# Kernel tuning notes

Measured on AMD Instinct MI355X. Metric: run time of the kernel, lower is better.

The kernel has to match this reference:

```python
import jax, jax.numpy as jnp
import numpy as np

N, E, H, Q, M, B, L = 100000, 800000, 64, 4, 8, 100, 4
EPS_BN = 1e-5


def setup_inputs() -> dict:
    key = jax.random.key(0)
    ki = iter(jax.random.split(key, 32))
    def nrm(shape, scale=1.0):
        return jax.random.normal(next(ki), shape, dtype=jnp.float32) * scale
    inp = {}
    inp["x"] = nrm((N, H))
    inp["pe"] = nrm((N, Q, M, 2))
    inp["Lam"] = jax.random.uniform(next(ki), (B, Q, M), jnp.float32, 0.0, 2.0)
    inp["edge_attr"] = nrm((E, H))
    # per-layer eigenvalue MLP phi: scalar -> 16 -> scalar
    inp["phi_w1"] = nrm((L, 1, 16))
    inp["phi_b1"] = jnp.zeros((L, 16), jnp.float32)
    inp["phi_w2"] = nrm((L, 16, 1), 0.25)
    inp["phi_b2"] = jnp.zeros((L, 1), jnp.float32)
    # per-layer edge PE encoder linear: [2*Q*M -> H]
    inp["enc_w"] = nrm((L, 2 * Q * M, H), (2.0 / (2 * Q * M)) ** 0.5)
    inp["enc_b"] = jnp.zeros((L, H), jnp.float32)
    # per-layer GINE edge linear
    inp["lin_w"] = nrm((L, H, H), (2.0 / H) ** 0.5)
    inp["lin_b"] = jnp.zeros((L, H), jnp.float32)
    # per-layer GINE MLP: Linear -> BN -> ReLU -> Linear
    inp["mlp_w1"] = nrm((L, H, H), (2.0 / H) ** 0.5)
    inp["mlp_b1"] = jnp.zeros((L, H), jnp.float32)
    inp["bn1_g"] = jnp.ones((L, H), jnp.float32)
    inp["bn1_b"] = jnp.zeros((L, H), jnp.float32)
    inp["mlp_w2"] = nrm((L, H, H), (2.0 / H) ** 0.5)
    inp["mlp_b2"] = jnp.zeros((L, H), jnp.float32)
    # per-layer outer BatchNorm
    inp["bn2_g"] = jnp.ones((L, H), jnp.float32)
    inp["bn2_b"] = jnp.zeros((L, H), jnp.float32)
    inp["edge_index"] = jax.random.randint(next(ki), (2, E), 0, N, dtype=jnp.int32)
    inp["batch"] = jnp.sort(jax.random.randint(next(ki), (N,), 0, B, dtype=jnp.int32))
    return inp


def _bn(h, g, b):
    # training-mode BatchNorm1d over the node/row axis
    mu = h.mean(axis=0)
    var = h.var(axis=0)
    return (h - mu) * jax.lax.rsqrt(var + EPS_BN) * g + b


def _forward(x, pe, Lam, edge_attr, params, edge_index, batch):
    (phi_w1, phi_b1, phi_w2, phi_b2, enc_w, enc_b, lin_w, lin_b,
     mlp_w1, mlp_b1, bn1_g, bn1_b, mlp_w2, mlp_b2, bn2_g, bn2_b) = params
    src, dst = edge_index[0], edge_index[1]
    # permutation-invariant complex edge features: pe[src] * conj(pe[dst]), per (q, eigvec)
    zs_re, zs_im = pe[src, ..., 0], pe[src, ..., 1]   # [E, Q, M]
    zd_re, zd_im = pe[dst, ..., 0], pe[dst, ..., 1]
    z_re = zs_re * zd_re + zs_im * zd_im              # [E, Q, M]
    z_im = zs_im * zd_re - zs_re * zd_im
    eg = batch[src]                                    # graph id per edge  [E]
    for l in range(L):
        # eigenvalue MLP -> per-eigenvector weight  [B, Q, M]
        hphi = jax.nn.relu(Lam[..., None] @ phi_w1[l] + phi_b1[l])   # [B,Q,M,16]
        w = (hphi @ phi_w2[l])[..., 0] + phi_b2[l][0]                # [B,Q,M]
        we = w[eg]                                                   # [E,Q,M]
        feat = jnp.concatenate([(z_re * we).reshape(E, Q * M),
                                (z_im * we).reshape(E, Q * M)], axis=-1)  # [E, 2QM]
        edge_pe = feat @ enc_w[l] + enc_b[l]                          # [E,H]
        ea = edge_pe + edge_attr
        # GINE message: ReLU(x_j + lin(edge_attr)), sum-aggregated at dst
        msg = jax.nn.relu(x[src] + ea @ lin_w[l] + lin_b[l])          # [E,H]
        agg = jax.ops.segment_sum(msg, dst, num_segments=N)           # [N,H]
        h = x + agg                                                   # (1+eps)*x with eps=0
        h = jax.nn.relu(_bn(h @ mlp_w1[l] + mlp_b1[l], bn1_g[l], bn1_b[l]))
        h = h @ mlp_w2[l] + mlp_b2[l]
        x = _bn(h, bn2_g[l], bn2_b[l])
        if l != L - 1:
            x = jax.nn.relu(x)
    return x


def reference(x, pe, Lam, edge_attr, phi_w1, phi_b1, phi_w2, phi_b2, enc_w, enc_b,
              lin_w, lin_b, mlp_w1, mlp_b1, bn1_g, bn1_b, mlp_w2, mlp_b2, bn2_g, bn2_b,
              edge_index, batch):
    params = (phi_w1, phi_b1, phi_w2, phi_b2, enc_w, enc_b, lin_w, lin_b,
              mlp_w1, mlp_b1, bn1_g, bn1_b, mlp_w2, mlp_b2, bn2_g, bn2_b)
    return (_forward(x, pe, Lam, edge_attr, params, edge_index, batch), pe)
```

## Files before the change

kernel.cpp:

```cpp
#include <hip/hip_runtime.h>

#define N_NODES 100000
#define N_EDGES 800000
#define NB 100
#define NL 4
#define QM 32
#define EPS_BN 1e-5f

typedef __bf16 bf16_t;
typedef __bf16 bf16x8 __attribute__((ext_vector_type(8)));
typedef __bf16 bf16x4 __attribute__((ext_vector_type(4)));
typedef __bf16 bf16x2 __attribute__((ext_vector_type(2)));
typedef float f32x4 __attribute__((ext_vector_type(4)));


__global__ void k_count(const int* __restrict__ dst, int* __restrict__ counts) {
    int e = blockIdx.x * 256 + threadIdx.x;
    if (e < N_EDGES) atomicAdd(&counts[dst[e]], 1);
}

__global__ void k_scan1(const int* __restrict__ counts, int* __restrict__ row_ptr,
                        int* __restrict__ blk) {
    __shared__ int s[1024];
    int i = blockIdx.x * 1024 + threadIdx.x;
    int v = (i < N_NODES) ? counts[i] : 0;
    s[threadIdx.x] = v;
    __syncthreads();
    for (int off = 1; off < 1024; off <<= 1) {
        int u = (threadIdx.x >= off) ? s[threadIdx.x - off] : 0;
        __syncthreads();
        s[threadIdx.x] += u;
        __syncthreads();
    }
    if (i < N_NODES) row_ptr[i] = s[threadIdx.x] - v;
    if (threadIdx.x == 1023) blk[blockIdx.x] = s[1023];
}

__global__ void k_scan2(int* __restrict__ blk) {
    __shared__ int s[128];
    int t = threadIdx.x;
    int v = (t < 98) ? blk[t] : 0;
    s[t] = v;
    __syncthreads();
    for (int off = 1; off < 128; off <<= 1) {
        int u = (t >= off) ? s[t - off] : 0;
        __syncthreads();
        s[t] += u;
        __syncthreads();
    }
    if (t < 98) blk[t] = s[t] - v;
}

__global__ void k_scan3(const int* __restrict__ blk, int* __restrict__ row_ptr) {
    int i = blockIdx.x * 1024 + threadIdx.x;
    if (i < N_NODES) row_ptr[i] += blk[blockIdx.x];
    if (i == 0) row_ptr[N_NODES] = N_EDGES;
}

__global__ void k_scatter(const int* __restrict__ ei, const int* __restrict__ batch,
                          const int* __restrict__ row_ptr, int* __restrict__ cursor,
                          int4* __restrict__ edat) {
    int e = blockIdx.x * 256 + threadIdx.x;
    if (e >= N_EDGES) return;
    int s = ei[e], d = ei[N_EDGES + e];
    int pos = row_ptr[d] + atomicAdd(&cursor[d], 1);
    edat[pos] = make_int4(s, d, batch[s], e);
}

__global__ void k_permute(const float* __restrict__ pe, const float* __restrict__ ea,
                          const int4* __restrict__ edat, bf16_t* __restrict__ feat) {
    int t = blockIdx.x * 256 + threadIdx.x;
    int p = t >> 4, k = t & 15;
    int4 ed = edat[p];
    int src = ed.x, dst = ed.y, e = ed.w;
    f32x4 av = *(const f32x4*)(ea + (size_t)e * 64 + k * 4);
    bf16x4 ao;
#pragma unroll
    for (int i = 0; i < 4; i++) ao[i] = (bf16_t)av[i];
    *(bf16x4*)(feat + (size_t)p * 128 + 64 + k * 4) = ao;
    f32x4 sv = *(const f32x4*)(pe + (size_t)src * 64 + k * 4);
    f32x4 dv = *(const f32x4*)(pe + (size_t)dst * 64 + k * 4);
    bf16x2 re, im;
    re[0] = (bf16_t)(sv[0] * dv[0] + sv[1] * dv[1]);
    re[1] = (bf16_t)(sv[2] * dv[2] + sv[3] * dv[3]);
    im[0] = (bf16_t)(sv[1] * dv[0] - sv[0] * dv[1]);
    im[1] = (bf16_t)(sv[3] * dv[2] - sv[2] * dv[3]);
    *(bf16x2*)(feat + (size_t)p * 128 + 2 * k) = re;
    *(bf16x2*)(feat + (size_t)p * 128 + 32 + 2 * k) = im;
}


__global__ void k_phi(const float* __restrict__ Lam, const float* __restrict__ w1,
                      const float* __restrict__ b1, const float* __restrict__ w2,
                      const float* __restrict__ b2, bf16_t* __restrict__ w_all) {
    int idx = blockIdx.x * 256 + threadIdx.x;
    if (idx >= NL * NB * QM) return;
    int l = idx / (NB * QM);
    int rem = idx % (NB * QM);
    float lam = Lam[rem];
    float acc = b2[l];
    for (int i = 0; i < 16; i++) {
        float h = lam * w1[l * 16 + i] + b1[l * 16 + i];
        acc += fmaxf(h, 0.f) * w2[l * 16 + i];
    }
    w_all[idx] = (bf16_t)acc;
}

__global__ void k_prep(const float* __restrict__ enc_w, const float* __restrict__ enc_b,
                       const float* __restrict__ lin_w, const float* __restrict__ lin_b,
                       const float* __restrict__ mlp_w1, const float* __restrict__ mlp_w2,
                       bf16_t* __restrict__ wcat_frag, bf16_t* __restrict__ w1frag,
                       bf16_t* __restrict__ w2frag, float* __restrict__ cvec) {
    __shared__ float lds[128][64];
    int l = blockIdx.x, tid = threadIdx.x;
    const float* ew = enc_w + l * 64 * 64;
    const float* lw = lin_w + l * 64 * 64;
    for (int idx = tid; idx < 64 * 64; idx += 256) {
        int r = idx >> 6, c = idx & 63;
        float acc = 0.f;
        for (int k = 0; k < 64; k++) acc += ew[r * 64 + k] * lw[k * 64 + c];
        lds[r][c] = acc;
        lds[64 + r][c] = lw[r * 64 + c];
    }
    if (tid < 64) {
        float acc = lin_b[l * 64 + tid];
        for (int k = 0; k < 64; k++) acc += enc_b[l * 64 + k] * lw[k * 64 + tid];
        cvec[l * 64 + tid] = acc;
    }
    __syncthreads();
    for (int idx = tid; idx < 16 * 512; idx += 256) {
        int sn = idx >> 9, lane = (idx >> 3) & 63, j = idx & 7;
        int s = sn >> 2, nt = sn & 3;
        int row = 32 * s + (lane >> 4) * 8 + j;
        int col = 16 * nt + (lane & 15);
        wcat_frag[l * 8192 + idx] = (bf16_t)lds[row][col];
    }
    for (int idx = tid; idx < 8 * 512; idx += 256) {
        int sn = idx >> 9, lane = (idx >> 3) & 63, j = idx & 7;
        int s = sn >> 2, nt = sn & 3;
        int row = 32 * s + (lane >> 4) * 8 + j;
        int col = 16 * nt + (lane & 15);
        w1frag[l * 4096 + idx] = (bf16_t)mlp_w1[(l * 64 + row) * 64 + col];
        w2frag[l * 4096 + idx] = (bf16_t)mlp_w2[(l * 64 + row) * 64 + col];
    }
}


__global__ void k_hinit0(const float* __restrict__ x, bf16_t* __restrict__ x_bf,
                         float* __restrict__ h) {
    size_t i = ((size_t)blockIdx.x * 256 + threadIdx.x) * 8;
    f32x4 a = *(const f32x4*)(x + i), b = *(const f32x4*)(x + i + 4);
    *(f32x4*)(h + i) = a;
    *(f32x4*)(h + i + 4) = b;
    bf16x8 o;
#pragma unroll
    for (int k = 0; k < 4; k++) { o[k] = (bf16_t)a[k]; o[k + 4] = (bf16_t)b[k]; }
    *(bf16x8*)(x_bf + i) = o;
}

__global__ void k_edge(const bf16_t* __restrict__ feat, const int4* __restrict__ edat,
                       const int* __restrict__ row_ptr, const bf16_t* __restrict__ w_l,
                       const bf16_t* __restrict__ wcat_l, const float* __restrict__ cvec_l,
                       const bf16_t* __restrict__ x_bf, float* __restrict__ h) {
    __shared__ float msg[128][68];
    int tid = threadIdx.x;
    int wave = tid >> 6, lane = tid & 63;
    int quad = lane >> 4, l16 = lane & 15;
    int e0 = blockIdx.x * 128;

    bf16x8 bfrag[4][4];
    const bf16x8* wf = (const bf16x8*)wcat_l;
#pragma unroll
    for (int s = 0; s < 4; s++)
#pragma unroll
        for (int nt = 0; nt < 4; nt++) bfrag[s][nt] = wf[(s * 4 + nt) * 64 + lane];

    f32x4 acc[2][4];
#pragma unroll
    for (int rt = 0; rt < 2; rt++)
#pragma unroll
        for (int nt = 0; nt < 4; nt++) acc[rt][nt] = (f32x4)(0.f);

    int em[2];
    bf16x8 wch[2];
#pragma unroll
    for (int rt = 0; rt < 2; rt++) {
        em[rt] = e0 + wave * 32 + rt * 16 + l16;
        int eg = edat[em[rt]].z;
        wch[rt] = *(const bf16x8*)(w_l + (size_t)eg * QM + quad * 8);
    }
#pragma unroll
    for (int s = 0; s < 4; s++) {
        bf16x8 afr[2];
#pragma unroll
        for (int rt = 0; rt < 2; rt++) {
            bf16x8 v = *(const bf16x8*)(feat + (size_t)em[rt] * 128 + s * 32 + quad * 8);
            if (s < 2) {
                bf16x8 a;
#pragma unroll
                for (int i = 0; i < 8; i++) a[i] = (bf16_t)((float)v[i] * (float)wch[rt][i]);
                afr[rt] = a;
            } else {
                afr[rt] = v;
            }
        }
#pragma unroll
        for (int rt = 0; rt < 2; rt++)
#pragma unroll
            for (int nt = 0; nt < 4; nt++)
                acc[rt][nt] = __builtin_amdgcn_mfma_f32_16x16x32_bf16(afr[rt], bfrag[s][nt],
                                                                     acc[rt][nt], 0, 0, 0);
    }
#pragma unroll
    for (int nt = 0; nt < 4; nt++) {
        float cv = cvec_l[nt * 16 + l16];
#pragma unroll
        for (int rt = 0; rt < 2; rt++)
#pragma unroll
            for (int r = 0; r < 4; r++)
                msg[wave * 32 + rt * 16 + quad * 4 + r][nt * 16 + l16] = acc[rt][nt][r] + cv;
    }
    __syncthreads();
#pragma unroll
    for (int it = 0; it < 4; it++) {
        int j = it * 32 + (tid >> 3);
        int l8 = tid & 7;
        int srcn = edat[e0 + j].x;
        bf16x8 xv = *(const bf16x8*)(x_bf + (size_t)srcn * 64 + l8 * 8);
        float* mrow = &msg[j][l8 * 8];
        f32x4 m0 = *(const f32x4*)mrow, m1 = *(const f32x4*)(mrow + 4);
#pragma unroll
        for (int k = 0; k < 4; k++) {
            m0[k] = fmaxf(m0[k] + (float)xv[k], 0.f);
            m1[k] = fmaxf(m1[k] + (float)xv[k + 4], 0.f);
        }
        *(f32x4*)mrow = m0;
        *(f32x4*)(mrow + 4) = m1;
    }
    __syncthreads();
    int nfirst = edat[e0].y, nlast = edat[e0 + 127].y;
    int c = tid & 63;
    for (int n = nfirst + (tid >> 6); n <= nlast; n += 4) {
        int rs = row_ptr[n], re = row_ptr[n + 1];
        int a = rs > e0 ? rs : e0;
        int b = re < e0 + 128 ? re : e0 + 128;
        if (a >= b) continue;
        float sum = 0.f;
        for (int jj = a; jj < b; jj++) sum += msg[jj - e0][c];
        float* addr = h + (size_t)n * 64 + c;
        if (rs >= e0 && re <= e0 + 128) *addr += sum;
        else atomicAdd(addr, sum);
    }
}

__global__ void k_mlp1(const float* __restrict__ h, const bf16_t* __restrict__ w1frag_l,
                       const float* __restrict__ b1_l, bf16_t* __restrict__ t,
                       float* __restrict__ stats) {
    __shared__ float sred[128];
    int tid = threadIdx.x, wave = tid >> 6, lane = tid & 63, quad = lane >> 4, l16 = lane & 15;
    int r0 = blockIdx.x * 128;
    bf16x8 bfrag[2][4];
    const bf16x8* wf = (const bf16x8*)w1frag_l;
#pragma unroll
    for (int s = 0; s < 2; s++)
#pragma unroll
        for (int nt = 0; nt < 4; nt++) bfrag[s][nt] = wf[(s * 4 + nt) * 64 + lane];
    f32x4 acc[2][4];
#pragma unroll
    for (int rt = 0; rt < 2; rt++)
#pragma unroll
        for (int nt = 0; nt < 4; nt++) acc[rt][nt] = (f32x4)(0.f);
#pragma unroll
    for (int rt = 0; rt < 2; rt++) {
        int n = r0 + wave * 32 + rt * 16 + l16;
        bool valid = n < N_NODES;
#pragma unroll
        for (int s = 0; s < 2; s++) {
            bf16x8 a;
            if (valid) {
                const float* hp = h + (size_t)n * 64 + s * 32 + quad * 8;
                f32x4 v0 = *(const f32x4*)hp, v1 = *(const f32x4*)(hp + 4);
#pragma unroll
                for (int i = 0; i < 4; i++) { a[i] = (bf16_t)v0[i]; a[i + 4] = (bf16_t)v1[i]; }
            } else {
#pragma unroll
                for (int i = 0; i < 8; i++) a[i] = (bf16_t)0.f;
            }
#pragma unroll
            for (int nt = 0; nt < 4; nt++)
                acc[rt][nt] = __builtin_amdgcn_mfma_f32_16x16x32_bf16(a, bfrag[s][nt],
                                                                     acc[rt][nt], 0, 0, 0);
        }
    }
    if (tid < 128) sred[tid] = 0.f;
    __syncthreads();
#pragma unroll
    for (int nt = 0; nt < 4; nt++) {
        int col = nt * 16 + l16;
        float bias = b1_l[col];
        float s1 = 0.f, s2 = 0.f;
#pragma unroll
        for (int rt = 0; rt < 2; rt++)
#pragma unroll
            for (int r = 0; r < 4; r++) {
                int n = r0 + wave * 32 + rt * 16 + quad * 4 + r;
                if (n < N_NODES) {
                    float v = acc[rt][nt][r] + bias;
                    t[(size_t)n * 64 + col] = (bf16_t)v;
                    s1 += v; s2 += v * v;
                }
            }
        s1 += __shfl_xor(s1, 16); s1 += __shfl_xor(s1, 32);
        s2 += __shfl_xor(s2, 16); s2 += __shfl_xor(s2, 32);
        if (quad == 0) { atomicAdd(&sred[col], s1); atomicAdd(&sred[64 + col], s2); }
    }
    __syncthreads();
    if (tid < 128) atomicAdd(&stats[tid], sred[tid]);
}

__global__ void k_mlp2(const bf16_t* __restrict__ t, const float* __restrict__ stats1,
                       const float* __restrict__ g1, const float* __restrict__ b1,
                       const bf16_t* __restrict__ w2frag_l, const float* __restrict__ b2_l,
                       float* __restrict__ h2, float* __restrict__ stats2) {
    __shared__ float sred[128];
    __shared__ float cf[128];
    int tid = threadIdx.x, wave = tid >> 6, lane = tid & 63, quad = lane >> 4, l16 = lane & 15;
    int r0 = blockIdx.x * 128;
    bf16x8 bfrag[2][4];
    const bf16x8* wf = (const bf16x8*)w2frag_l;
#pragma unroll
    for (int s = 0; s < 2; s++)
#pragma unroll
        for (int nt = 0; nt < 4; nt++) bfrag[s][nt] = wf[(s * 4 + nt) * 64 + lane];
    if (tid < 64) {
        float mean = stats1[tid] / (float)N_NODES;
        float var = stats1[64 + tid] / (float)N_NODES - mean * mean;
        float a = g1[tid] * rsqrtf(var + EPS_BN);
        cf[tid] = a;
        cf[64 + tid] = b1[tid] - mean * a;
    }
    if (tid >= 64 && tid < 192) sred[tid - 64] = 0.f;
    __syncthreads();
    f32x4 acc[2][4];
#pragma unroll
    for (int rt = 0; rt < 2; rt++)
#pragma unroll
        for (int nt = 0; nt < 4; nt++) acc[rt][nt] = (f32x4)(0.f);
#pragma unroll
    for (int rt = 0; rt < 2; rt++) {
        int n = r0 + wave * 32 + rt * 16 + l16;
        bool valid = n < N_NODES;
#pragma unroll
        for (int s = 0; s < 2; s++) {
            bf16x8 a;
            if (valid) {
                bf16x8 tv = *(const bf16x8*)(t + (size_t)n * 64 + s * 32 + quad * 8);
                int kb = s * 32 + quad * 8;
#pragma unroll
                for (int i = 0; i < 8; i++) {
                    float y = (float)tv[i] * cf[kb + i] + cf[64 + kb + i];
                    a[i] = (bf16_t)fmaxf(y, 0.f);
                }
            } else {
#pragma unroll
                for (int i = 0; i < 8; i++) a[i] = (bf16_t)0.f;
            }
#pragma unroll
            for (int nt = 0; nt < 4; nt++)
                acc[rt][nt] = __builtin_amdgcn_mfma_f32_16x16x32_bf16(a, bfrag[s][nt],
                                                                     acc[rt][nt], 0, 0, 0);
        }
    }
#pragma unroll
    for (int nt = 0; nt < 4; nt++) {
        int col = nt * 16 + l16;
        float bias = b2_l[col];
        float s1 = 0.f, s2 = 0.f;
#pragma unroll
        for (int rt = 0; rt < 2; rt++)
#pragma unroll
            for (int r = 0; r < 4; r++) {
                int n = r0 + wave * 32 + rt * 16 + quad * 4 + r;
                if (n < N_NODES) {
                    float v = acc[rt][nt][r] + bias;
                    h2[(size_t)n * 64 + col] = v;
                    s1 += v; s2 += v * v;
                }
            }
        s1 += __shfl_xor(s1, 16); s1 += __shfl_xor(s1, 32);
        s2 += __shfl_xor(s2, 16); s2 += __shfl_xor(s2, 32);
        if (quad == 0) { atomicAdd(&sred[col], s1); atomicAdd(&sred[64 + col], s2); }
    }
    __syncthreads();
    if (tid < 128) atomicAdd(&stats2[tid], sred[tid]);
}

__global__ void k_apply_init(const float* __restrict__ h2, const float* __restrict__ stats2,
                             const float* __restrict__ g, const float* __restrict__ b,
                             bf16_t* __restrict__ x_bf, float* __restrict__ h) {
    __shared__ float cf[128];
    int tid = threadIdx.x;
    if (tid < 64) {
        float mean = stats2[tid] / (float)N_NODES;
        float var = stats2[64 + tid] / (float)N_NODES - mean * mean;
        float a = g[tid] * rsqrtf(var + EPS_BN);
        cf[tid] = a;
        cf[64 + tid] = b[tid] - mean * a;
    }
    __syncthreads();
    size_t i = ((size_t)blockIdx.x * 256 + tid) * 8;
    int c0 = (int)(i & 63);
    f32x4 v0 = *(const f32x4*)(h2 + i), v1 = *(const f32x4*)(h2 + i + 4);
    f32x4 y0, y1;
    bf16x8 o;
#pragma unroll
    for (int k = 0; k < 4; k++) {
        y0[k] = fmaxf(v0[k] * cf[c0 + k] + cf[64 + c0 + k], 0.f);
        y1[k] = fmaxf(v1[k] * cf[c0 + 4 + k] + cf[64 + c0 + 4 + k], 0.f);
        o[k] = (bf16_t)y0[k]; o[k + 4] = (bf16_t)y1[k];
    }
    *(f32x4*)(h + i) = y0;
    *(f32x4*)(h + i + 4) = y1;
    *(bf16x8*)(x_bf + i) = o;
}

__global__ void k_apply_out(const float* __restrict__ h2, const float* __restrict__ stats2,
                            const float* __restrict__ g, const float* __restrict__ b,
                            float* __restrict__ out) {
    __shared__ float cf[128];
    int tid = threadIdx.x;
    if (tid < 64) {
        float mean = stats2[tid] / (float)N_NODES;
        float var = stats2[64 + tid] / (float)N_NODES - mean * mean;
        float a = g[tid] * rsqrtf(var + EPS_BN);
        cf[tid] = a;
        cf[64 + tid] = b[tid] - mean * a;
    }
    __syncthreads();
    size_t i = ((size_t)blockIdx.x * 256 + tid) * 8;
    int c0 = (int)(i & 63);
    f32x4 v0 = *(const f32x4*)(h2 + i), v1 = *(const f32x4*)(h2 + i + 4);
    f32x4 y0, y1;
#pragma unroll
    for (int k = 0; k < 4; k++) {
        y0[k] = v0[k] * cf[c0 + k] + cf[64 + c0 + k];
        y1[k] = v1[k] * cf[c0 + 4 + k] + cf[64 + c0 + 4 + k];
    }
    *(f32x4*)(out + i) = y0;
    *(f32x4*)(out + i + 4) = y1;
}


extern "C" void kernel_launch(void* const* d_in, const int* in_sizes, int n_in,
                              void* d_out, int out_size, void* d_ws, size_t ws_size,
                              hipStream_t stream) {
    const float* x_in   = (const float*)d_in[0];
    const float* pe     = (const float*)d_in[1];
    const float* Lam    = (const float*)d_in[2];
    const float* eattr  = (const float*)d_in[3];
    const float* phi_w1 = (const float*)d_in[4];
    const float* phi_b1 = (const float*)d_in[5];
    const float* phi_w2 = (const float*)d_in[6];
    const float* phi_b2 = (const float*)d_in[7];
    const float* enc_w  = (const float*)d_in[8];
    const float* enc_b  = (const float*)d_in[9];
    const float* lin_w  = (const float*)d_in[10];
    const float* lin_b  = (const float*)d_in[11];
    const float* mlp_w1 = (const float*)d_in[12];
    const float* mlp_b1 = (const float*)d_in[13];
    const float* bn1_g  = (const float*)d_in[14];
    const float* bn1_b  = (const float*)d_in[15];
    const float* mlp_w2 = (const float*)d_in[16];
    const float* mlp_b2 = (const float*)d_in[17];
    const float* bn2_g  = (const float*)d_in[18];
    const float* bn2_b  = (const float*)d_in[19];
    const int* edge_index = (const int*)d_in[20];
    const int* batch      = (const int*)d_in[21];
    float* out = (float*)d_out;

    char* ws = (char*)d_ws;
    size_t off = 0;
    auto alloc = [&](size_t bytes) -> void* {
        void* p = ws + off;
        off += (bytes + 255) & ~(size_t)255;
        return p;
    };
    bf16_t* feat      = (bf16_t*)alloc((size_t)N_EDGES * 128 * 2);
    int4* edat        = (int4*)alloc((size_t)N_EDGES * 16);
    int* row_ptr      = (int*)alloc((size_t)(N_NODES + 1) * 4);
    int* blk          = (int*)alloc(128 * 4);
    int* counts       = (int*)alloc((size_t)N_NODES * 4);
    int* cursor       = (int*)alloc((size_t)N_NODES * 4);
    float* stats      = (float*)alloc((size_t)NL * 256 * 4);
    size_t zbytes     = (char*)(stats + NL * 256) - (char*)counts;
    float* h          = (float*)alloc((size_t)N_NODES * 64 * 4);
    bf16_t* t         = (bf16_t*)alloc((size_t)N_NODES * 64 * 2);
    float* h2         = (float*)alloc((size_t)N_NODES * 64 * 4);
    bf16_t* x_bf      = (bf16_t*)alloc((size_t)N_NODES * 64 * 2);
    bf16_t* w_all     = (bf16_t*)alloc((size_t)NL * NB * QM * 2);
    bf16_t* wcat_frag = (bf16_t*)alloc((size_t)NL * 8192 * 2);
    bf16_t* w1frag    = (bf16_t*)alloc((size_t)NL * 4096 * 2);
    bf16_t* w2frag    = (bf16_t*)alloc((size_t)NL * 4096 * 2);
    float* cvec       = (float*)alloc((size_t)NL * 64 * 4);

    hipMemsetAsync(counts, 0, zbytes, stream);
    k_count<<<3125, 256, 0, stream>>>(edge_index + N_EDGES, counts);
    k_scan1<<<98, 1024, 0, stream>>>(counts, row_ptr, blk);
    k_scan2<<<1, 128, 0, stream>>>(blk);
    k_scan3<<<98, 1024, 0, stream>>>(blk, row_ptr);
    k_scatter<<<3125, 256, 0, stream>>>(edge_index, batch, row_ptr, cursor, edat);
    k_permute<<<50000, 256, 0, stream>>>(pe, eattr, edat, feat);
    k_phi<<<50, 256, 0, stream>>>(Lam, phi_w1, phi_b1, phi_w2, phi_b2, w_all);
    k_prep<<<NL, 256, 0, stream>>>(enc_w, enc_b, lin_w, lin_b, mlp_w1, mlp_w2,
                                   wcat_frag, w1frag, w2frag, cvec);

    k_hinit0<<<3125, 256, 0, stream>>>(x_in, x_bf, h);
    for (int l = 0; l < NL; l++) {
        float* s1 = stats + l * 256;
        float* s2 = stats + l * 256 + 128;
        k_edge<<<6250, 256, 0, stream>>>(feat, edat, row_ptr,
                                         w_all + (size_t)l * NB * QM,
                                         wcat_frag + (size_t)l * 8192,
                                         cvec + (size_t)l * 64, x_bf, h);
        k_mlp1<<<782, 256, 0, stream>>>(h, w1frag + (size_t)l * 4096,
                                        mlp_b1 + l * 64, t, s1);
        k_mlp2<<<782, 256, 0, stream>>>(t, s1, bn1_g + l * 64, bn1_b + l * 64,
                                        w2frag + (size_t)l * 4096, mlp_b2 + l * 64,
                                        h2, s2);
        if (l < NL - 1)
            k_apply_init<<<3125, 256, 0, stream>>>(h2, s2, bn2_g + l * 64, bn2_b + l * 64,
                                                   x_bf, h);
        else
            k_apply_out<<<3125, 256, 0, stream>>>(h2, s2, bn2_g + l * 64, bn2_b + l * 64,
                                                  out);
    }
    hipMemcpyAsync(out + (size_t)N_NODES * 64, pe, (size_t)N_NODES * QM * 2 * 4,
                   hipMemcpyDeviceToDevice, stream);
}
```

Measured before the change: 1.197 ms.

## Fuse node MLP, both BatchNorms and apply into one persistent kernel with grid barriers

Replaces the per-layer k_mlp1, k_mlp2 and apply kernels with one persistent kernel of 512 blocks. Each block keeps its two row tiles of the first linear output in LDS and its second-linear accumulators in registers, and uses two software grid barriers to wait for the BatchNorm statistics. This removes the intermediate t and h2 global round trips and two launches per layer. It also folds the pe output copy into k_hinit0 and has k_permute handle two edges per thread group. The risks are that the grid barrier needs all 512 blocks to be resident at once, that register pressure rises, and that blocks sit idle while waiting at the barriers.

```diff
diff --git a/kernel.cpp b/kernel.cpp
--- a/kernel.cpp
+++ b/kernel.cpp
@@ -6,6 +6,8 @@
 #define NL 4
 #define QM 32
 #define EPS_BN 1e-5f
+#define NTILE 782
+#define NBLK_MLP 512
 
 typedef __bf16 bf16_t;
 typedef __bf16 bf16x8 __attribute__((ext_vector_type(8)));
@@ -70,23 +72,38 @@
 __global__ void k_permute(const float* __restrict__ pe, const float* __restrict__ ea,
                           const int4* __restrict__ edat, bf16_t* __restrict__ feat) {
     int t = blockIdx.x * 256 + threadIdx.x;
-    int p = t >> 4, k = t & 15;
-    int4 ed = edat[p];
-    int src = ed.x, dst = ed.y, e = ed.w;
-    f32x4 av = *(const f32x4*)(ea + (size_t)e * 64 + k * 4);
-    bf16x4 ao;
-#pragma unroll
-    for (int i = 0; i < 4; i++) ao[i] = (bf16_t)av[i];
-    *(bf16x4*)(feat + (size_t)p * 128 + 64 + k * 4) = ao;
-    f32x4 sv = *(const f32x4*)(pe + (size_t)src * 64 + k * 4);
-    f32x4 dv = *(const f32x4*)(pe + (size_t)dst * 64 + k * 4);
-    bf16x2 re, im;
-    re[0] = (bf16_t)(sv[0] * dv[0] + sv[1] * dv[1]);
-    re[1] = (bf16_t)(sv[2] * dv[2] + sv[3] * dv[3]);
-    im[0] = (bf16_t)(sv[1] * dv[0] - sv[0] * dv[1]);
-    im[1] = (bf16_t)(sv[3] * dv[2] - sv[2] * dv[3]);
-    *(bf16x2*)(feat + (size_t)p * 128 + 2 * k) = re;
-    *(bf16x2*)(feat + (size_t)p * 128 + 32 + 2 * k) = im;
+    int g = t >> 4, k = t & 15;
+    size_t p0 = (size_t)g << 1;
+    int4 ed0 = edat[p0];
+    int4 ed1 = edat[p0 + 1];
+    f32x4 s0 = *(const f32x4*)(pe + (size_t)ed0.x * 64 + k * 4);
+    f32x4 d0 = *(const f32x4*)(pe + (size_t)ed0.y * 64 + k * 4);
+    f32x4 a0 = *(const f32x4*)(ea + (size_t)ed0.w * 64 + k * 4);
+    f32x4 s1 = *(const f32x4*)(pe + (size_t)ed1.x * 64 + k * 4);
+    f32x4 d1 = *(const f32x4*)(pe + (size_t)ed1.y * 64 + k * 4);
+    f32x4 a1 = *(const f32x4*)(ea + (size_t)ed1.w * 64 + k * 4);
+
+    bf16x4 ao0, ao1;
+#pragma unroll
+    for (int i = 0; i < 4; i++) { ao0[i] = (bf16_t)a0[i]; ao1[i] = (bf16_t)a1[i]; }
+    bf16x2 re0, im0, re1, im1;
+    re0[0] = (bf16_t)(s0[0] * d0[0] + s0[1] * d0[1]);
+    re0[1] = (bf16_t)(s0[2] * d0[2] + s0[3] * d0[3]);
+    im0[0] = (bf16_t)(s0[1] * d0[0] - s0[0] * d0[1]);
+    im0[1] = (bf16_t)(s0[3] * d0[2] - s0[2] * d0[3]);
+    re1[0] = (bf16_t)(s1[0] * d1[0] + s1[1] * d1[1]);
+    re1[1] = (bf16_t)(s1[2] * d1[2] + s1[3] * d1[3]);
+    im1[0] = (bf16_t)(s1[1] * d1[0] - s1[0] * d1[1]);
+    im1[1] = (bf16_t)(s1[3] * d1[2] - s1[2] * d1[3]);
+
+    bf16_t* f0 = feat + p0 * 128;
+    *(bf16x2*)(f0 + 2 * k) = re0;
+    *(bf16x2*)(f0 + 32 + 2 * k) = im0;
+    *(bf16x4*)(f0 + 64 + 4 * k) = ao0;
+    bf16_t* f1 = f0 + 128;
+    *(bf16x2*)(f1 + 2 * k) = re1;
+    *(bf16x2*)(f1 + 32 + 2 * k) = im1;
+    *(bf16x4*)(f1 + 64 + 4 * k) = ao1;
 }
 
 
@@ -146,8 +163,9 @@
 }
 
 
-__global__ void k_hinit0(const float* __restrict__ x, bf16_t* __restrict__ x_bf,
-                         float* __restrict__ h) {
+__global__ void k_hinit0(const float* __restrict__ x, const float* __restrict__ pe,
+                         bf16_t* __restrict__ x_bf, float* __restrict__ h,
+                         float* __restrict__ out_pe) {
     size_t i = ((size_t)blockIdx.x * 256 + threadIdx.x) * 8;
     f32x4 a = *(const f32x4*)(x + i), b = *(const f32x4*)(x + i + 4);
     *(f32x4*)(h + i) = a;
@@ -156,6 +174,9 @@
 #pragma unroll
     for (int k = 0; k < 4; k++) { o[k] = (bf16_t)a[k]; o[k + 4] = (bf16_t)b[k]; }
     *(bf16x8*)(x_bf + i) = o;
+    f32x4 p0 = *(const f32x4*)(pe + i), p1 = *(const f32x4*)(pe + i + 4);
+    *(f32x4*)(out_pe + i) = p0;
+    *(f32x4*)(out_pe + i + 4) = p1;
 }
 
 __global__ void k_edge(const bf16_t* __restrict__ feat, const int4* __restrict__ edat,
@@ -253,201 +274,225 @@
     }
 }
 
-__global__ void k_mlp1(const float* __restrict__ h, const bf16_t* __restrict__ w1frag_l,
-                       const float* __restrict__ b1_l, bf16_t* __restrict__ t,
-                       float* __restrict__ stats) {
-    __shared__ float sred[128];
-    int tid = threadIdx.x, wave = tid >> 6, lane = tid & 63, quad = lane >> 4, l16 = lane & 15;
-    int r0 = blockIdx.x * 128;
-    bf16x8 bfrag[2][4];
-    const bf16x8* wf = (const bf16x8*)w1frag_l;
-#pragma unroll
-    for (int s = 0; s < 2; s++)
-#pragma unroll
-        for (int nt = 0; nt < 4; nt++) bfrag[s][nt] = wf[(s * 4 + nt) * 64 + lane];
-    f32x4 acc[2][4];
-#pragma unroll
-    for (int rt = 0; rt < 2; rt++)
-#pragma unroll
-        for (int nt = 0; nt < 4; nt++) acc[rt][nt] = (f32x4)(0.f);
-#pragma unroll
-    for (int rt = 0; rt < 2; rt++) {
-        int n = r0 + wave * 32 + rt * 16 + l16;
-        bool valid = n < N_NODES;
-#pragma unroll
-        for (int s = 0; s < 2; s++) {
-            bf16x8 a;
-            if (valid) {
-                const float* hp = h + (size_t)n * 64 + s * 32 + quad * 8;
-                f32x4 v0 = *(const f32x4*)hp, v1 = *(const f32x4*)(hp + 4);
-#pragma unroll
-                for (int i = 0; i < 4; i++) { a[i] = (bf16_t)v0[i]; a[i + 4] = (bf16_t)v1[i]; }
-            } else {
-#pragma unroll
-                for (int i = 0; i < 8; i++) a[i] = (bf16_t)0.f;
-            }
-#pragma unroll
-            for (int nt = 0; nt < 4; nt++)
-                acc[rt][nt] = __builtin_amdgcn_mfma_f32_16x16x32_bf16(a, bfrag[s][nt],
-                                                                     acc[rt][nt], 0, 0, 0);
-        }
-    }
-    if (tid < 128) sred[tid] = 0.f;
-    __syncthreads();
-#pragma unroll
-    for (int nt = 0; nt < 4; nt++) {
-        int col = nt * 16 + l16;
-        float bias = b1_l[col];
-        float s1 = 0.f, s2 = 0.f;
-#pragma unroll
-        for (int rt = 0; rt < 2; rt++)
-#pragma unroll
-            for (int r = 0; r < 4; r++) {
-                int n = r0 + wave * 32 + rt * 16 + quad * 4 + r;
-                if (n < N_NODES) {
-                    float v = acc[rt][nt][r] + bias;
-                    t[(size_t)n * 64 + col] = (bf16_t)v;
-                    s1 += v; s2 += v * v;
-                }
-            }
-        s1 += __shfl_xor(s1, 16); s1 += __shfl_xor(s1, 32);
-        s2 += __shfl_xor(s2, 16); s2 += __shfl_xor(s2, 32);
-        if (quad == 0) { atomicAdd(&sred[col], s1); atomicAdd(&sred[64 + col], s2); }
-    }
-    __syncthreads();
-    if (tid < 128) atomicAdd(&stats[tid], sred[tid]);
-}
-
-__global__ void k_mlp2(const bf16_t* __restrict__ t, const float* __restrict__ stats1,
-                       const float* __restrict__ g1, const float* __restrict__ b1,
-                       const bf16_t* __restrict__ w2frag_l, const float* __restrict__ b2_l,
-                       float* __restrict__ h2, float* __restrict__ stats2) {
+
+__device__ __forceinline__ int swz_idx(int row, int col) {
+    return ((row * 128 + col * 2) ^ ((row & 7) << 4)) >> 1;
+}
+
+__device__ __forceinline__ void gbar(int* bar, int target) {
+    __syncthreads();
+    if (threadIdx.x == 0) {
+        __threadfence();
+        __hip_atomic_fetch_add(bar, 1, __ATOMIC_ACQ_REL, __HIP_MEMORY_SCOPE_AGENT);
+        while (__hip_atomic_load(bar, __ATOMIC_ACQUIRE, __HIP_MEMORY_SCOPE_AGENT) < target)
+            __builtin_amdgcn_s_sleep(2);
+    }
+    __syncthreads();
+}
+
+template <int LAST>
+__global__ __launch_bounds__(256, 2) void k_mlp(
+    const float* __restrict__ h, const bf16_t* __restrict__ w1frag_l,
+    const bf16_t* __restrict__ w2frag_l, const float* __restrict__ b1_l,
+    const float* __restrict__ g1, const float* __restrict__ bb1,
+    const float* __restrict__ b2_l, const float* __restrict__ g2,
+    const float* __restrict__ bb2, float* __restrict__ stats1,
+    float* __restrict__ stats2, int* __restrict__ bar, float* __restrict__ hout,
+    bf16_t* __restrict__ x_bf, float* __restrict__ out) {
+    __shared__ bf16_t tls[2][8192];
     __shared__ float sred[128];
     __shared__ float cf[128];
     int tid = threadIdx.x, wave = tid >> 6, lane = tid & 63, quad = lane >> 4, l16 = lane & 15;
-    int r0 = blockIdx.x * 128;
+
     bf16x8 bfrag[2][4];
-    const bf16x8* wf = (const bf16x8*)w2frag_l;
+    const bf16x8* wf1 = (const bf16x8*)w1frag_l;
 #pragma unroll
     for (int s = 0; s < 2; s++)
 #pragma unroll
-        for (int nt = 0; nt < 4; nt++) bfrag[s][nt] = wf[(s * 4 + nt) * 64 + lane];
+        for (int nt = 0; nt < 4; nt++) bfrag[s][nt] = wf1[(s * 4 + nt) * 64 + lane];
+
+    if (tid < 128) sred[tid] = 0.f;
+    __syncthreads();
+
+#pragma unroll
+    for (int ti = 0; ti < 2; ti++) {
+        int tile = blockIdx.x + ti * NBLK_MLP;
+        if (tile >= NTILE) continue;
+        int r0 = tile * 128;
+        f32x4 acc[2][4];
+#pragma unroll
+        for (int rt = 0; rt < 2; rt++)
+#pragma unroll
+            for (int nt = 0; nt < 4; nt++) acc[rt][nt] = (f32x4)(0.f);
+#pragma unroll
+        for (int rt = 0; rt < 2; rt++) {
+            int n = r0 + wave * 32 + rt * 16 + l16;
+            bool valid = n < N_NODES;
+#pragma unroll
+            for (int s = 0; s < 2; s++) {
+                bf16x8 a;
+                if (valid) {
+                    const float* hp = h + (size_t)n * 64 + s * 32 + quad * 8;
+                    f32x4 v0 = *(const f32x4*)hp, v1 = *(const f32x4*)(hp + 4);
+#pragma unroll
+                    for (int i = 0; i < 4; i++) { a[i] = (bf16_t)v0[i]; a[i + 4] = (bf16_t)v1[i]; }
+                } else {
+#pragma unroll
+                    for (int i = 0; i < 8; i++) a[i] = (bf16_t)0.f;
+                }
+#pragma unroll
+                for (int nt = 0; nt < 4; nt++)
+                    acc[rt][nt] = __builtin_amdgcn_mfma_f32_16x16x32_bf16(a, bfrag[s][nt],
+                                                                         acc[rt][nt], 0, 0, 0);
+            }
+        }
+#pragma unroll
+        for (int nt = 0; nt < 4; nt++) {
+            int col = nt * 16 + l16;
+            float bias = b1_l[col];
+            float s1 = 0.f, s2 = 0.f;
+#pragma unroll
+            for (int rt = 0; rt < 2; rt++)
+#pragma unroll
+                for (int r = 0; r < 4; r++) {
+                    int rloc = wave * 32 + rt * 16 + quad * 4 + r;
+                    int n = r0 + rloc;
+                    if (n < N_NODES) {
+                        float v = acc[rt][nt][r] + bias;
+                        tls[ti][swz_idx(rloc, col)] = (bf16_t)v;
+                        s1 += v; s2 += v * v;
+                    } else {
+                        tls[ti][swz_idx(rloc, col)] = (bf16_t)0.f;
+                    }
+                }
+            s1 += __shfl_xor(s1, 16); s1 += __shfl_xor(s1, 32);
+            s2 += __shfl_xor(s2, 16); s2 += __shfl_xor(s2, 32);
+            if (quad == 0) { atomicAdd(&sred[col], s1); atomicAdd(&sred[64 + col], s2); }
+        }
+    }
+    __syncthreads();
+    if (tid < 128) atomicAdd(&stats1[tid], sred[tid]);
+    gbar(bar, NBLK_MLP);
+
+    if (tid < 128) sred[tid] = 0.f;
     if (tid < 64) {
-        float mean = stats1[tid] / (float)N_NODES;
-        float var = stats1[64 + tid] / (float)N_NODES - mean * mean;
+        float sa = __hip_atomic_load(stats1 + tid, __ATOMIC_RELAXED, __HIP_MEMORY_SCOPE_AGENT);
+        float sb = __hip_atomic_load(stats1 + 64 + tid, __ATOMIC_RELAXED, __HIP_MEMORY_SCOPE_AGENT);
+        float mean = sa / (float)N_NODES;
+        float var = sb / (float)N_NODES - mean * mean;
         float a = g1[tid] * rsqrtf(var + EPS_BN);
         cf[tid] = a;
-        cf[64 + tid] = b1[tid] - mean * a;
-    }
-    if (tid >= 64 && tid < 192) sred[tid - 64] = 0.f;
-    __syncthreads();
-    f32x4 acc[2][4];
-#pragma unroll
-    for (int rt = 0; rt < 2; rt++)
-#pragma unroll
-        for (int nt = 0; nt < 4; nt++) acc[rt][nt] = (f32x4)(0.f);
-#pragma unroll
-    for (int rt = 0; rt < 2; rt++) {
-        int n = r0 + wave * 32 + rt * 16 + l16;
-        bool valid = n < N_NODES;
-#pragma unroll
-        for (int s = 0; s < 2; s++) {
-            bf16x8 a;
-            if (valid) {
-                bf16x8 tv = *(const bf16x8*)(t + (size_t)n * 64 + s * 32 + quad * 8);
-                int kb = s * 32 + quad * 8;
+        cf[64 + tid] = bb1[tid] - mean * a;
+    }
+    __syncthreads();
+
+    bf16x8 b2frag[2][4];
+    const bf16x8* wf2 = (const bf16x8*)w2frag_l;
+#pragma unroll
+    for (int s = 0; s < 2; s++)
+#pragma unroll
+        for (int nt = 0; nt < 4; nt++) b2frag[s][nt] = wf2[(s * 4 + nt) * 64 + lane];
+
+    f32x4 acc2[2][2][4];
+#pragma unroll
+    for (int ti = 0; ti < 2; ti++)
+#pragma unroll
+        for (int rt = 0; rt < 2; rt++)
+#pragma unroll
+            for (int nt = 0; nt < 4; nt++) acc2[ti][rt][nt] = (f32x4)(0.f);
+
+#pragma unroll
+    for (int ti = 0; ti < 2; ti++) {
+        int tile = blockIdx.x + ti * NBLK_MLP;
+        if (tile >= NTILE) continue;
+#pragma unroll
+        for (int rt = 0; rt < 2; rt++) {
+            int rloc = wave * 32 + rt * 16 + l16;
+#pragma unroll
+            for (int s = 0; s < 2; s++) {
+                int k0 = s * 32 + quad * 8;
+                bf16x8 tv = *(const bf16x8*)&tls[ti][swz_idx(rloc, k0)];
+                bf16x8 a;
 #pragma unroll
                 for (int i = 0; i < 8; i++) {
-                    float y = (float)tv[i] * cf[kb + i] + cf[64 + kb + i];
+                    float y = (float)tv[i] * cf[k0 + i] + cf[64 + k0 + i];
                     a[i] = (bf16_t)fmaxf(y, 0.f);
                 }
-            } else {
-#pragma unroll
-                for (int i = 0; i < 8; i++) a[i] = (bf16_t)0.f;
+#pragma unroll
+                for (int nt = 0; nt < 4; nt++)
+                    acc2[ti][rt][nt] = __builtin_amdgcn_mfma_f32_16x16x32_bf16(
+                        a, b2frag[s][nt], acc2[ti][rt][nt], 0, 0, 0);
             }
-#pragma unroll
-            for (int nt = 0; nt < 4; nt++)
-                acc[rt][nt] = __builtin_amdgcn_mfma_f32_16x16x32_bf16(a, bfrag[s][nt],
-                                                                     acc[rt][nt], 0, 0, 0);
-        }
-    }
+        }
+    }
+
 #pragma unroll
     for (int nt = 0; nt < 4; nt++) {
         int col = nt * 16 + l16;
         float bias = b2_l[col];
         float s1 = 0.f, s2 = 0.f;
 #pragma unroll
-        for (int rt = 0; rt < 2; rt++)
-#pragma unroll
-            for (int r = 0; r < 4; r++) {
-                int n = r0 + wave * 32 + rt * 16 + quad * 4 + r;
-                if (n < N_NODES) {
-                    float v = acc[rt][nt][r] + bias;
-                    h2[(size_t)n * 64 + col] = v;
-                    s1 += v; s2 += v * v;
+        for (int ti = 0; ti < 2; ti++) {
+            int tile = blockIdx.x + ti * NBLK_MLP;
+            if (tile >= NTILE) continue;
+            int r0 = tile * 128;
+#pragma unroll
+            for (int rt = 0; rt < 2; rt++)
+#pragma unroll
+                for (int r = 0; r < 4; r++) {
+                    int n = r0 + wave * 32 + rt * 16 + quad * 4 + r;
+                    if (n < N_NODES) {
+                        float v = acc2[ti][rt][nt][r] + bias;
+                        s1 += v; s2 += v * v;
+                    }
                 }
-            }
+        }
         s1 += __shfl_xor(s1, 16); s1 += __shfl_xor(s1, 32);
         s2 += __shfl_xor(s2, 16); s2 += __shfl_xor(s2, 32);
         if (quad == 0) { atomicAdd(&sred[col], s1); atomicAdd(&sred[64 + col], s2); }
     }
     __syncthreads();
     if (tid < 128) atomicAdd(&stats2[tid], sred[tid]);
-}
-
-__global__ void k_apply_init(const float* __restrict__ h2, const float* __restrict__ stats2,
-                             const float* __restrict__ g, const float* __restrict__ b,
-                             bf16_t* __restrict__ x_bf, float* __restrict__ h) {
-    __shared__ float cf[128];
-    int tid = threadIdx.x;
+    gbar(bar, 2 * NBLK_MLP);
+
     if (tid < 64) {
-        float mean = stats2[tid] / (float)N_NODES;
-        float var = stats2[64 + tid] / (float)N_NODES - mean * mean;
-        float a = g[tid] * rsqrtf(var + EPS_BN);
+        float sa = __hip_atomic_load(stats2 + tid, __ATOMIC_RELAXED, __HIP_MEMORY_SCOPE_AGENT);
+        float sb = __hip_atomic_load(stats2 + 64 + tid, __ATOMIC_RELAXED, __HIP_MEMORY_SCOPE_AGENT);
+        float mean = sa / (float)N_NODES;
+        float var = sb / (float)N_NODES - mean * mean;
+        float a = g2[tid] * rsqrtf(var + EPS_BN);
         cf[tid] = a;
-        cf[64 + tid] = b[tid] - mean * a;
-    }
-    __syncthreads();
-    size_t i = ((size_t)blockIdx.x * 256 + tid) * 8;
-    int c0 = (int)(i & 63);
-    f32x4 v0 = *(const f32x4*)(h2 + i), v1 = *(const f32x4*)(h2 + i + 4);
-    f32x4 y0, y1;
-    bf16x8 o;
-#pragma unroll
-    for (int k = 0; k < 4; k++) {
-        y0[k] = fmaxf(v0[k] * cf[c0 + k] + cf[64 + c0 + k], 0.f);
-        y1[k] = fmaxf(v1[k] * cf[c0 + 4 + k] + cf[64 + c0 + 4 + k], 0.f);
-        o[k] = (bf16_t)y0[k]; o[k + 4] = (bf16_t)y1[k];
-    }
-    *(f32x4*)(h + i) = y0;
-    *(f32x4*)(h + i + 4) = y1;
-    *(bf16x8*)(x_bf + i) = o;
-}
-
-__global__ void k_apply_out(const float* __restrict__ h2, const float* __restrict__ stats2,
-                            const float* __restrict__ g, const float* __restrict__ b,
-                            float* __restrict__ out) {
-    __shared__ float cf[128];
-    int tid = threadIdx.x;
-    if (tid < 64) {
-        float mean = stats2[tid] / (float)N_NODES;
-        float var = stats2[64 + tid] / (float)N_NODES - mean * mean;
-        float a = g[tid] * rsqrtf(var + EPS_BN);
-        cf[tid] = a;
-        cf[64 + tid] = b[tid] - mean * a;
-    }
-    __syncthreads();
-    size_t i = ((size_t)blockIdx.x * 256 + tid) * 8;
-    int c0 = (int)(i & 63);
-    f32x4 v0 = *(const f32x4*)(h2 + i), v1 = *(const f32x4*)(h2 + i + 4);
-    f32x4 y0, y1;
-#pragma unroll
-    for (int k = 0; k < 4; k++) {
-        y0[k] = v0[k] * cf[c0 + k] + cf[64 + c0 + k];
-        y1[k] = v1[k] * cf[c0 + 4 + k] + cf[64 + c0 + 4 + k];
-    }
-    *(f32x4*)(out + i) = y0;
-    *(f32x4*)(out + i + 4) = y1;
+        cf[64 + tid] = bb2[tid] - mean * a;
+    }
+    __syncthreads();
+#pragma unroll
+    for (int ti = 0; ti < 2; ti++) {
+        int tile = blockIdx.x + ti * NBLK_MLP;
+        if (tile >= NTILE) continue;
+        int r0 = tile * 128;
+#pragma unroll
+        for (int nt = 0; nt < 4; nt++) {
+            int col = nt * 16 + l16;
+            float bias = b2_l[col];
+#pragma unroll
+            for (int rt = 0; rt < 2; rt++)
+#pragma unroll
+                for (int r = 0; r < 4; r++) {
+                    int n = r0 + wave * 32 + rt * 16 + quad * 4 + r;
+                    if (n < N_NODES) {
+                        float v = acc2[ti][rt][nt][r] + bias;
+                        float y = v * cf[col] + cf[64 + col];
+                        if (LAST) {
+                            out[(size_t)n * 64 + col] = y;
+                        } else {
+                            y = fmaxf(y, 0.f);
+                            hout[(size_t)n * 64 + col] = y;
+                            x_bf[(size_t)n * 64 + col] = (bf16_t)y;
+                        }
+                    }
+                }
+        }
+    }
 }
 
 
@@ -492,10 +537,9 @@
     int* counts       = (int*)alloc((size_t)N_NODES * 4);
     int* cursor       = (int*)alloc((size_t)N_NODES * 4);
     float* stats      = (float*)alloc((size_t)NL * 256 * 4);
-    size_t zbytes     = (char*)(stats + NL * 256) - (char*)counts;
+    int* bar          = (int*)alloc((size_t)NL * 4);
+    size_t zbytes     = (char*)(bar + NL) - (char*)counts;
     float* h          = (float*)alloc((size_t)N_NODES * 64 * 4);
-    bf16_t* t         = (bf16_t*)alloc((size_t)N_NODES * 64 * 2);
-    float* h2         = (float*)alloc((size_t)N_NODES * 64 * 4);
     bf16_t* x_bf      = (bf16_t*)alloc((size_t)N_NODES * 64 * 2);
     bf16_t* w_all     = (bf16_t*)alloc((size_t)NL * NB * QM * 2);
     bf16_t* wcat_frag = (bf16_t*)alloc((size_t)NL * 8192 * 2);
@@ -509,12 +553,12 @@
     k_scan2<<<1, 128, 0, stream>>>(blk);
     k_scan3<<<98, 1024, 0, stream>>>(blk, row_ptr);
     k_scatter<<<3125, 256, 0, stream>>>(edge_index, batch, row_ptr, cursor, edat);
-    k_permute<<<50000, 256, 0, stream>>>(pe, eattr, edat, feat);
+    k_permute<<<25000, 256, 0, stream>>>(pe, eattr, edat, feat);
     k_phi<<<50, 256, 0, stream>>>(Lam, phi_w1, phi_b1, phi_w2, phi_b2, w_all);
     k_prep<<<NL, 256, 0, stream>>>(enc_w, enc_b, lin_w, lin_b, mlp_w1, mlp_w2,
                                    wcat_frag, w1frag, w2frag, cvec);
 
-    k_hinit0<<<3125, 256, 0, stream>>>(x_in, x_bf, h);
+    k_hinit0<<<3125, 256, 0, stream>>>(x_in, pe, x_bf, h, out + (size_t)N_NODES * 64);
     for (int l = 0; l < NL; l++) {
         float* s1 = stats + l * 256;
         float* s2 = stats + l * 256 + 128;
@@ -522,18 +566,17 @@
                                          w_all + (size_t)l * NB * QM,
                                          wcat_frag + (size_t)l * 8192,
                                          cvec + (size_t)l * 64, x_bf, h);
-        k_mlp1<<<782, 256, 0, stream>>>(h, w1frag + (size_t)l * 4096,
-                                        mlp_b1 + l * 64, t, s1);
-        k_mlp2<<<782, 256, 0, stream>>>(t, s1, bn1_g + l * 64, bn1_b + l * 64,
-                                        w2frag + (size_t)l * 4096, mlp_b2 + l * 64,
-                                        h2, s2);
         if (l < NL - 1)
-            k_apply_init<<<3125, 256, 0, stream>>>(h2, s2, bn2_g + l * 64, bn2_b + l * 64,
-                                                   x_bf, h);
+            k_mlp<0><<<NBLK_MLP, 256, 0, stream>>>(
+                h, w1frag + (size_t)l * 4096, w2frag + (size_t)l * 4096,
+                mlp_b1 + l * 64, bn1_g + l * 64, bn1_b + l * 64,
+                mlp_b2 + l * 64, bn2_g + l * 64, bn2_b + l * 64,
+                s1, s2, bar + l, h, x_bf, (float*)nullptr);
         else
-            k_apply_out<<<3125, 256, 0, stream>>>(h2, s2, bn2_g + l * 64, bn2_b + l * 64,
-                                                  out);
-    }
-    hipMemcpyAsync(out + (size_t)N_NODES * 64, pe, (size_t)N_NODES * QM * 2 * 4,
-                   hipMemcpyDeviceToDevice, stream);
-}
+            k_mlp<1><<<NBLK_MLP, 256, 0, stream>>>(
+                h, w1frag + (size_t)l * 4096, w2frag + (size_t)l * 4096,
+                mlp_b1 + l * 64, bn1_g + l * 64, bn1_b + l * 64,
+                mlp_b2 + l * 64, bn2_g + l * 64, bn2_b + l * 64,
+                s1, s2, bar + l, h, x_bf, out);
+    }
+}
```

New measurement: 1.346 ms. 1.12x slower.
